# Kernel tuning notes

Hardware: AMD Instinct MI355X
Metric: run time of the kernel (lower is better)

Reference implementation:

```python
import jax, jax.numpy as jnp
import numpy as np

SX, SY, C, K = 256, 256, 3, 15
DD, DT, SIGMA = 5, 0.2, 0.65
C0 = tuple(i % C for i in range(K))
C1 = tuple(tuple(i for i in range(K) if i % C == c) for c in range(C))
MA = DD - SIGMA  # flow magnitude bound


def _sobel(A):
    # A: (X, Y, c) -> (X, Y, 2, c); matches jsp.signal.convolve2d(..., mode='same')
    kx = jnp.array([[1., 0., -1.], [2., 0., -2.], [1., 0., -1.]], dtype=A.dtype)
    ky = kx.T
    # convolve2d flips the kernel; emulate true convolution by correlating with rot180 kernels
    kern = jnp.stack([jnp.rot90(ky, 2), jnp.rot90(kx, 2)])[:, None]  # (2,1,3,3): [grad_y, grad_x]
    x = jnp.transpose(A, (2, 0, 1))[:, None]                          # (c,1,X,Y)
    out = jax.lax.conv_general_dilated(x, kern, (1, 1), 'SAME')       # (c,2,X,Y)
    return jnp.transpose(out, (2, 3, 1, 0))                           # (X,Y,2,c)


def _reintegration(A, P, F):
    # Reintegration tracking, has_hidden=True, border='wall', mix='softmax'
    xs, ys = jnp.meshgrid(jnp.arange(SX), jnp.arange(SY))
    pos = (jnp.dstack((ys, xs)) + .5).astype(A.dtype)     # (X,Y,2) cell centers (row, col)
    mus = pos[..., None] + jnp.clip(DT * F, -MA, MA)      # (X,Y,2,C) target centers
    mus = jnp.clip(mus, SIGMA, SX - SIGMA)                # wall border
    shifts = jnp.array([(dx, dy) for dx in range(-DD, DD + 1) for dy in range(-DD, DD + 1)])
    cap = min(1., 2 * SIGMA)

    def step(sft):
        sh = (sft[0], sft[1])
        Ar = jnp.roll(A, sh, axis=(0, 1))
        Pr = jnp.roll(P, sh, axis=(0, 1))
        mur = jnp.roll(mus, sh, axis=(0, 1))
        dpmu = jnp.abs(pos[..., None] - mur)              # (X,Y,2,C)
        sz = .5 - dpmu + SIGMA
        area = jnp.prod(jnp.clip(sz, 0., cap), axis=2) / (4 * SIGMA ** 2)  # (X,Y,C)
        return Ar * area, Pr

    nA, nP = jax.vmap(step)(shifts)                       # (N,X,Y,C), (N,X,Y,K)
    expnA = jnp.exp(nA.sum(-1, keepdims=True)) - 1.       # softmax mix rule
    newA = nA.sum(0)
    newP = (nP * expnA).sum(0) / (expnA.sum(0) + 1e-10)
    return newA, newP


def _forward(A, P, fK_real, fK_imag, m, s):
    fK = fK_real + 1j * fK_imag                           # (X,Y,K) kernel FFTs
    fA = jnp.fft.fft2(A, axes=(0, 1))                     # (X,Y,C)
    fAk = jnp.take(fA, jnp.array(C0), axis=2)             # (X,Y,K) per-kernel source channel
    U = jnp.real(jnp.fft.ifft2(fK * fAk, axes=(0, 1)))    # (X,Y,K)
    U = (2. * jnp.exp(-((U - m) ** 2) / (2. * s ** 2)) - 1.) * P  # growth(U,m,s)*P
    U = jnp.dstack([U[:, :, C1[c]].sum(-1) for c in range(C)])    # (X,Y,C)
    F = _sobel(U)                                         # (X,Y,2,C)
    Cg = _sobel(A.sum(-1, keepdims=True))                 # (X,Y,2,1)
    alpha = jnp.clip((A[:, :, None, :] / 2.) ** 2, 0., 1.)
    F = jnp.clip(F * (1. - alpha) - Cg * alpha, -MA, MA)
    return _reintegration(A, P, F)


def setup_inputs() -> dict:
    key = jax.random.key(0)
    kA, kP, kr, km, ks, ka, kb, kw = jax.random.split(key, 8)
    A = jax.random.uniform(kA, (SX, SY, C), dtype=jnp.float32)
    P = jax.random.uniform(kP, (SX, SY, K), dtype=jnp.float32)
    R = 15.0
    r = jax.random.uniform(kr, (K,), minval=.2, maxval=1.)
    m = jax.random.uniform(km, (K,), minval=.05, maxval=.5, dtype=jnp.float32)
    s = jax.random.uniform(ks, (K,), minval=.001, maxval=.18, dtype=jnp.float32)
    a = jax.random.uniform(ka, (K, 3))
    b = jax.random.uniform(kb, (K, 3), minval=.001, maxval=1.)
    w = jax.random.uniform(kw, (K, 3), minval=.01, maxval=.5)
    mid = SX // 2
    D = jnp.linalg.norm(jnp.mgrid[-mid:mid, -mid:mid], axis=0)[..., None] / ((R + 15.) * r)  # (X,Y,K)
    Kk = jax.nn.sigmoid(-(D - 1.) * 10.) * (b * jnp.exp(-((D[..., None] - a) / w) ** 2)).sum(-1)
    nK = Kk / Kk.sum((0, 1), keepdims=True)
    fK = jnp.fft.fft2(jnp.fft.fftshift(nK, axes=(0, 1)), axes=(0, 1))
    return {"A": A, "P": P,
            "fK_real": jnp.real(fK).astype(jnp.float32),
            "fK_imag": jnp.imag(fK).astype(jnp.float32),
            "m": m, "s": s}


def reference(A, P, fK_real, fK_imag, m, s):
    return _forward(A, P, fK_real, fK_imag, m, s)
```

## Files before the change

### kernel.cpp

```cpp
#include <hip/hip_runtime.h>


#define XY  65536
#define NC  3
#define NK  15
#define WPAD 260

__device__ __forceinline__ float2 cmul(float2 a, float2 b) {
  return make_float2(a.x * b.x - a.y * b.y, a.x * b.y + a.y * b.x);
}

__device__ __forceinline__ void fft256_lds(float2* b0, float2* b1, int t, float sign) {
  float2* src = b0;
  float2* dst = b1;
#pragma unroll
  for (int stage = 0; stage < 4; ++stage) {
    __syncthreads();
    const int Ns = 1 << (2 * stage);
    float2 v0 = src[t];
    float2 v1 = src[t + 64];
    float2 v2 = src[t + 128];
    float2 v3 = src[t + 192];
    const int jm = t & (Ns - 1);
    float ang = sign * 6.283185307179586f * (float)jm / (float)(Ns * 4);
    float sn, cs;
    __sincosf(ang, &sn, &cs);
    float2 w1 = make_float2(cs, sn);
    float2 w2 = cmul(w1, w1);
    float2 w3 = cmul(w2, w1);
    v1 = cmul(v1, w1);
    v2 = cmul(v2, w2);
    v3 = cmul(v3, w3);
    float2 a0 = make_float2(v0.x + v2.x, v0.y + v2.y);
    float2 a1 = make_float2(v0.x - v2.x, v0.y - v2.y);
    float2 a2 = make_float2(v1.x + v3.x, v1.y + v3.y);
    float2 a3 = make_float2(v1.x - v3.x, v1.y - v3.y);
    float2 ia3 = make_float2(-sign * a3.y, sign * a3.x);
    const int idxD = ((t >> (2 * stage)) << (2 * stage)) * 4 + jm;
    dst[idxD]          = make_float2(a0.x + a2.x, a0.y + a2.y);
    dst[idxD + Ns]     = make_float2(a1.x + ia3.x, a1.y + ia3.y);
    dst[idxD + 2 * Ns] = make_float2(a0.x - a2.x, a0.y - a2.y);
    dst[idxD + 3 * Ns] = make_float2(a1.x - ia3.x, a1.y - ia3.y);
    float2* tmp = src; src = dst; dst = tmp;
  }
  __syncthreads();
}

__global__ __launch_bounds__(64) void k_rowfft(const float* __restrict__ A,
                                               float2* __restrict__ RF) {
  __shared__ float2 b0[256], b1[256];
  const int t = threadIdx.x;
  const int x = blockIdx.x & 255;
  const int c = blockIdx.x >> 8;
#pragma unroll
  for (int r = 0; r < 4; ++r) {
    int y = t + 64 * r;
    b0[y] = make_float2(A[(x * 256 + y) * NC + c], 0.0f);
  }
  fft256_lds(b0, b1, t, -1.0f);
#pragma unroll
  for (int r = 0; r < 4; ++r) {
    int y = t + 64 * r;
    RF[(c * 256 + x) * 256 + y] = b0[y];
  }
}

__global__ __launch_bounds__(512, 1) void k_colfft(const float* __restrict__ fKr,
                                                   const float* __restrict__ fKi,
                                                   const float2* __restrict__ RF,
                                                   float2* __restrict__ T2) {
  __shared__ float2 lds0[8 * WPAD];
  __shared__ float2 lds1[8 * WPAD];
  const int tid = threadIdx.x;
  const int k = blockIdx.x >> 5;
  const int y0 = (blockIdx.x & 31) << 3;
  const int c = k % 3;

  {
    const int q = tid & 3;
#pragma unroll
    for (int r = 0; r < 2; ++r) {
      const int x = (tid >> 2) + (r << 7);
      const float4* src = (const float4*)(RF + (c * XY + x * 256 + y0));
      float4 v = src[q];
      lds0[(2 * q) * WPAD + x]     = make_float2(v.x, v.y);
      lds0[(2 * q + 1) * WPAD + x] = make_float2(v.z, v.w);
    }
  }

  const int w = tid >> 6, lane = tid & 63;
  float2* b0 = lds0 + w * WPAD;
  float2* b1 = lds1 + w * WPAD;
  fft256_lds(b0, b1, lane, -1.0f);

  const int y = y0 + w;
  float2 fa[4];
#pragma unroll
  for (int r = 0; r < 4; ++r) fa[r] = b0[lane + 64 * r];
#pragma unroll
  for (int r = 0; r < 4; ++r) {
    const int x = lane + 64 * r;
    const int fi = (x * 256 + y) * NK + k;
    float2 Kv = make_float2(fKr[fi], fKi[fi]);
    b0[x] = cmul(Kv, fa[r]);
  }
  fft256_lds(b0, b1, lane, 1.0f);

  {
    const int q = tid & 3;
#pragma unroll
    for (int r = 0; r < 2; ++r) {
      const int x = (tid >> 2) + (r << 7);
      float2 v0 = lds0[(2 * q) * WPAD + x];
      float2 v1 = lds0[(2 * q + 1) * WPAD + x];
      float4* dst = (float4*)(T2 + (k * XY + x * 256 + y0));
      dst[q] = make_float4(v0.x, v0.y, v1.x, v1.y);
    }
  }
}

__global__ __launch_bounds__(320, 1) void k_irowfft_growth(const float2* __restrict__ T2,
                                                           const float* __restrict__ P,
                                                           const float* __restrict__ m,
                                                           const float* __restrict__ s,
                                                           float* __restrict__ Ucol) {
  __shared__ float2 lds0[5 * WPAD];
  __shared__ float2 lds1[5 * WPAD];
  __shared__ float accs[5 * WPAD];
  const int tid = threadIdx.x;
  const int x = blockIdx.x & 255;
  const int c = blockIdx.x >> 8;
  const int j = tid >> 6, lane = tid & 63;
  const int k = c + 3 * j;

  float2* b0 = lds0 + j * WPAD;
  float2* b1 = lds1 + j * WPAD;
  const float2* src = T2 + (k * XY + x * 256);
#pragma unroll
  for (int r = 0; r < 4; ++r) {
    int y = lane + 64 * r;
    b0[y] = src[y];
  }
  fft256_lds(b0, b1, lane, 1.0f);

  const float mk = m[k];
  const float sk = s[k];
  const float inv2s2 = 0.5f / (sk * sk);
#pragma unroll
  for (int r = 0; r < 4; ++r) {
    int y = lane + 64 * r;
    float U = b0[y].x * (1.0f / 65536.0f);
    float d = U - mk;
    float g = 2.0f * __expf(-d * d * inv2s2) - 1.0f;
    accs[j * WPAD + y] = g * P[(x * 256 + y) * NK + k];
  }
  __syncthreads();
  if (tid < 256) {
    float sum = 0.f;
#pragma unroll
    for (int j2 = 0; j2 < 5; ++j2) sum += accs[j2 * WPAD + tid];
    Ucol[c * XY + x * 256 + tid] = sum;
  }
}

__global__ __launch_bounds__(256) void k_flow(const float* __restrict__ A,
                                              const float* __restrict__ Ucol,
                                              float* __restrict__ F) {
  const int idx = blockIdx.x * 256 + threadIdx.x;
  const int x = idx >> 8;
  const int y = idx & 255;
  const float MA = 4.35f;

  float u[3][3][3];
  float asum[3][3];
#pragma unroll
  for (int di = -1; di <= 1; ++di) {
#pragma unroll
    for (int dj = -1; dj <= 1; ++dj) {
      int xi = x + di, yj = y + dj;
      bool inb = ((unsigned)xi < 256u) && ((unsigned)yj < 256u);
      float a0 = 0.f, a1 = 0.f, a2 = 0.f, as = 0.f;
      if (inb) {
        int b = xi * 256 + yj;
        a0 = Ucol[0 * XY + b];
        a1 = Ucol[1 * XY + b];
        a2 = Ucol[2 * XY + b];
        const float* ap = A + b * NC;
        as = ap[0] + ap[1] + ap[2];
      }
      u[0][di + 1][dj + 1] = a0;
      u[1][di + 1][dj + 1] = a1;
      u[2][di + 1][dj + 1] = a2;
      asum[di + 1][dj + 1] = as;
    }
  }
  float cg0 = (asum[2][0] + 2.f * asum[2][1] + asum[2][2]) -
              (asum[0][0] + 2.f * asum[0][1] + asum[0][2]);
  float cg1 = (asum[0][2] + 2.f * asum[1][2] + asum[2][2]) -
              (asum[0][0] + 2.f * asum[1][0] + asum[2][0]);
  const int b = x * 256 + y;
#pragma unroll
  for (int c = 0; c < NC; ++c) {
    float f0 = (u[c][2][0] + 2.f * u[c][2][1] + u[c][2][2]) -
               (u[c][0][0] + 2.f * u[c][0][1] + u[c][0][2]);
    float f1 = (u[c][0][2] + 2.f * u[c][1][2] + u[c][2][2]) -
               (u[c][0][0] + 2.f * u[c][1][0] + u[c][2][0]);
    float ah = A[b * NC + c] * 0.5f;
    float al = fminf(ah * ah, 1.0f);
    f0 = fminf(fmaxf(f0 * (1.f - al) - cg0 * al, -MA), MA);
    f1 = fminf(fmaxf(f1 * (1.f - al) - cg1 * al, -MA), MA);
    F[(b * 2 + 0) * NC + c] = f0;
    F[(b * 2 + 1) * NC + c] = f1;
  }
}

__global__ __launch_bounds__(256) void k_reint(const float* __restrict__ A,
                                               const float* __restrict__ P,
                                               const float* __restrict__ F,
                                               float* __restrict__ outA,
                                               float* __restrict__ outP) {
  const int idx = blockIdx.x * 256 + threadIdx.x;
  const int x = idx >> 8;
  const int y = idx & 255;
  const float SIGMA = 0.65f;
  const float INV4S2 = 1.0f / (4.0f * 0.65f * 0.65f);
  const float DT = 0.2f;
  const float px = x + 0.5f;
  const float py = y + 0.5f;

  float accA[3] = {0.f, 0.f, 0.f};
  float accP[15];
#pragma unroll
  for (int k = 0; k < NK; ++k) accP[k] = 0.f;
  float esum = 0.f;

  for (int dx = -2; dx <= 2; ++dx) {
    for (int dy = -2; dy <= 2; ++dy) {
      const int sx = (x - dx) & 255;
      const int sy = (y - dy) & 255;
      const int sb = sx * 256 + sy;
      const float spx = sx + 0.5f;
      const float spy = sy + 0.5f;
      float sumnA = 0.f;
      float nAc[3];
#pragma unroll
      for (int c = 0; c < NC; ++c) {
        float f0 = F[(sb * 2 + 0) * NC + c];
        float f1 = F[(sb * 2 + 1) * NC + c];
        float mu0 = fminf(fmaxf(spx + DT * f0, SIGMA), 256.f - SIGMA);
        float mu1 = fminf(fmaxf(spy + DT * f1, SIGMA), 256.f - SIGMA);
        float sz0 = 0.5f - fabsf(px - mu0) + SIGMA;
        float sz1 = 0.5f - fabsf(py - mu1) + SIGMA;
        sz0 = fminf(fmaxf(sz0, 0.f), 1.f);
        sz1 = fminf(fmaxf(sz1, 0.f), 1.f);
        float area = sz0 * sz1 * INV4S2;
        float na = A[sb * NC + c] * area;
        nAc[c] = na;
        sumnA += na;
      }
      float e = __expf(sumnA) - 1.0f;
      accA[0] += nAc[0];
      accA[1] += nAc[1];
      accA[2] += nAc[2];
      esum += e;
      const float* pp = P + sb * NK;
#pragma unroll
      for (int k = 0; k < NK; ++k) accP[k] += pp[k] * e;
    }
  }
  const int b = x * 256 + y;
#pragma unroll
  for (int c = 0; c < NC; ++c) outA[b * NC + c] = accA[c];
  const float inv = 1.0f / (esum + 1e-10f);
#pragma unroll
  for (int k = 0; k < NK; ++k) outP[b * NK + k] = accP[k] * inv;
}

extern "C" void kernel_launch(void* const* d_in, const int* in_sizes, int n_in,
                              void* d_out, int out_size, void* d_ws, size_t ws_size,
                              hipStream_t stream) {
  const float* A   = (const float*)d_in[0];
  const float* P   = (const float*)d_in[1];
  const float* fKr = (const float*)d_in[2];
  const float* fKi = (const float*)d_in[3];
  const float* m   = (const float*)d_in[4];
  const float* s   = (const float*)d_in[5];

  float* ws = (float*)d_ws;
  float2* RF   = (float2*)ws;
  float2* T2   = RF + NC * XY;
  float*  Ucol = (float*)(T2 + NK * XY);
  float*  F    = Ucol + NC * XY;

  float* outA = (float*)d_out;
  float* outP = outA + NC * XY;

  k_rowfft<<<NC * 256, 64, 0, stream>>>(A, RF);
  k_colfft<<<NK * 32, 512, 0, stream>>>(fKr, fKi, RF, T2);
  k_irowfft_growth<<<NC * 256, 320, 0, stream>>>(T2, P, m, s, Ucol);
  k_flow<<<256, 256, 0, stream>>>(A, Ucol, F);
  k_reint<<<256, 256, 0, stream>>>(A, P, F, outA, outP);
}
```

Baseline: 107.4 us.

## Use wave-level fences in FFTs, prefetch operands, split reintegration across two threads

Each 256-point FFT is handled by a single wave, so the block-wide barriers between stages become wave barriers with compiler memory fences. Explicit __syncthreads are kept only where data crosses waves. Kernel-spectrum and P loads are hoisted ahead of the FFTs so their global latency overlaps compute. The reintegration kernel now splits each pixel's 25-neighbour gather across two lanes combined with shuffles, doubling the thread count. This relies on LDS ordering within a single wave holding correctly without a block barrier.

```diff
diff --git a/kernel.cpp b/kernel.cpp
--- a/kernel.cpp
+++ b/kernel.cpp
@@ -10,12 +10,18 @@
   return make_float2(a.x * b.x - a.y * b.y, a.x * b.y + a.y * b.x);
 }
 
-__device__ __forceinline__ void fft256_lds(float2* b0, float2* b1, int t, float sign) {
+__device__ __forceinline__ void wave_fence() {
+  asm volatile("" ::: "memory");
+  __builtin_amdgcn_wave_barrier();
+  asm volatile("" ::: "memory");
+}
+
+__device__ __forceinline__ void fft256_wave(float2* b0, float2* b1, int t, float sign) {
   float2* src = b0;
   float2* dst = b1;
 #pragma unroll
   for (int stage = 0; stage < 4; ++stage) {
-    __syncthreads();
+    wave_fence();
     const int Ns = 1 << (2 * stage);
     float2 v0 = src[t];
     float2 v1 = src[t + 64];
@@ -43,7 +49,7 @@
     dst[idxD + 3 * Ns] = make_float2(a1.x - ia3.x, a1.y - ia3.y);
     float2* tmp = src; src = dst; dst = tmp;
   }
-  __syncthreads();
+  wave_fence();
 }
 
 __global__ __launch_bounds__(64) void k_rowfft(const float* __restrict__ A,
@@ -57,7 +63,7 @@
     int y = t + 64 * r;
     b0[y] = make_float2(A[(x * 256 + y) * NC + c], 0.0f);
   }
-  fft256_lds(b0, b1, t, -1.0f);
+  fft256_wave(b0, b1, t, -1.0f);
 #pragma unroll
   for (int r = 0; r < 4; ++r) {
     int y = t + 64 * r;
@@ -75,6 +81,16 @@
   const int k = blockIdx.x >> 5;
   const int y0 = (blockIdx.x & 31) << 3;
   const int c = k % 3;
+  const int w = tid >> 6, lane = tid & 63;
+  const int y = y0 + w;
+
+  float2 Kv[4];
+#pragma unroll
+  for (int r = 0; r < 4; ++r) {
+    const int xx = lane + 64 * r;
+    const int fi = (xx * 256 + y) * NK + k;
+    Kv[r] = make_float2(fKr[fi], fKi[fi]);
+  }
 
   {
     const int q = tid & 3;
@@ -87,24 +103,22 @@
       lds0[(2 * q + 1) * WPAD + x] = make_float2(v.z, v.w);
     }
   }
-
-  const int w = tid >> 6, lane = tid & 63;
+  __syncthreads();
+
   float2* b0 = lds0 + w * WPAD;
   float2* b1 = lds1 + w * WPAD;
-  fft256_lds(b0, b1, lane, -1.0f);
-
-  const int y = y0 + w;
+  fft256_wave(b0, b1, lane, -1.0f);
+
   float2 fa[4];
 #pragma unroll
   for (int r = 0; r < 4; ++r) fa[r] = b0[lane + 64 * r];
 #pragma unroll
   for (int r = 0; r < 4; ++r) {
     const int x = lane + 64 * r;
-    const int fi = (x * 256 + y) * NK + k;
-    float2 Kv = make_float2(fKr[fi], fKi[fi]);
-    b0[x] = cmul(Kv, fa[r]);
-  }
-  fft256_lds(b0, b1, lane, 1.0f);
+    b0[x] = cmul(Kv[r], fa[r]);
+  }
+  fft256_wave(b0, b1, lane, 1.0f);
+  __syncthreads();
 
   {
     const int q = tid & 3;
@@ -133,6 +147,16 @@
   const int j = tid >> 6, lane = tid & 63;
   const int k = c + 3 * j;
 
+  float pv[4];
+#pragma unroll
+  for (int r = 0; r < 4; ++r) {
+    int y = lane + 64 * r;
+    pv[r] = P[(x * 256 + y) * NK + k];
+  }
+  const float mk = m[k];
+  const float sk = s[k];
+  const float inv2s2 = 0.5f / (sk * sk);
+
   float2* b0 = lds0 + j * WPAD;
   float2* b1 = lds1 + j * WPAD;
   const float2* src = T2 + (k * XY + x * 256);
@@ -141,18 +165,15 @@
     int y = lane + 64 * r;
     b0[y] = src[y];
   }
-  fft256_lds(b0, b1, lane, 1.0f);
-
-  const float mk = m[k];
-  const float sk = s[k];
-  const float inv2s2 = 0.5f / (sk * sk);
+  fft256_wave(b0, b1, lane, 1.0f);
+
 #pragma unroll
   for (int r = 0; r < 4; ++r) {
     int y = lane + 64 * r;
     float U = b0[y].x * (1.0f / 65536.0f);
     float d = U - mk;
     float g = 2.0f * __expf(-d * d * inv2s2) - 1.0f;
-    accs[j * WPAD + y] = g * P[(x * 256 + y) * NK + k];
+    accs[j * WPAD + y] = g * pv[r];
   }
   __syncthreads();
   if (tid < 256) {
@@ -219,9 +240,11 @@
                                                const float* __restrict__ F,
                                                float* __restrict__ outA,
                                                float* __restrict__ outP) {
-  const int idx = blockIdx.x * 256 + threadIdx.x;
-  const int x = idx >> 8;
-  const int y = idx & 255;
+  const int t = blockIdx.x * 256 + threadIdx.x;
+  const int pix = t >> 1;
+  const int half = t & 1;
+  const int x = pix >> 8;
+  const int y = pix & 255;
   const float SIGMA = 0.65f;
   const float INV4S2 = 1.0f / (4.0f * 0.65f * 0.65f);
   const float DT = 0.2f;
@@ -234,8 +257,12 @@
   for (int k = 0; k < NK; ++k) accP[k] = 0.f;
   float esum = 0.f;
 
-  for (int dx = -2; dx <= 2; ++dx) {
-    for (int dy = -2; dy <= 2; ++dy) {
+#pragma unroll
+  for (int i = 0; i < 13; ++i) {
+    const int cell = half * 13 + i;
+    if (cell < 25) {
+      const int dx = cell / 5 - 2;
+      const int dy = cell % 5 - 2;
       const int sx = (x - dx) & 255;
       const int sy = (y - dy) & 255;
       const int sb = sx * 256 + sy;
@@ -268,12 +295,22 @@
       for (int k = 0; k < NK; ++k) accP[k] += pp[k] * e;
     }
   }
-  const int b = x * 256 + y;
-#pragma unroll
-  for (int c = 0; c < NC; ++c) outA[b * NC + c] = accA[c];
-  const float inv = 1.0f / (esum + 1e-10f);
-#pragma unroll
-  for (int k = 0; k < NK; ++k) outP[b * NK + k] = accP[k] * inv;
+
+  esum += __shfl_xor(esum, 1);
+#pragma unroll
+  for (int c = 0; c < NC; ++c) accA[c] += __shfl_xor(accA[c], 1);
+#pragma unroll
+  for (int k = 0; k < NK; ++k) accP[k] += __shfl_xor(accP[k], 1);
+
+  const int b = pix;
+  if (half == 0) {
+#pragma unroll
+    for (int c = 0; c < NC; ++c) outA[b * NC + c] = accA[c];
+  } else {
+    const float inv = 1.0f / (esum + 1e-10f);
+#pragma unroll
+    for (int k = 0; k < NK; ++k) outP[b * NK + k] = accP[k] * inv;
+  }
 }
 
 extern "C" void kernel_launch(void* const* d_in, const int* in_sizes, int n_in,
@@ -299,5 +336,5 @@
   k_colfft<<<NK * 32, 512, 0, stream>>>(fKr, fKi, RF, T2);
   k_irowfft_growth<<<NC * 256, 320, 0, stream>>>(T2, P, m, s, Ucol);
   k_flow<<<256, 256, 0, stream>>>(A, Ucol, F);
-  k_reint<<<256, 256, 0, stream>>>(A, P, F, outA, outP);
-}
+  k_reint<<<512, 256, 0, stream>>>(A, P, F, outA, outP);
+}
```

New measurement: 111.5 us. 1.04x slower.
